# Kernel tuning notes

Measured on AMD Instinct MI355X. Metric: run time of the kernel, lower is better.

## Reference

```python
import jax, jax.numpy as jnp
import numpy as np
import math

B, MSA, L, D = 1, 64, 256, 512
H = 8
DH = D // H  # 64


def setup_inputs() -> dict:
    key = jax.random.key(0)
    ks = jax.random.split(key, 6)
    x = jax.random.normal(ks[0], (B, MSA, L, D), dtype=jnp.float32)
    Wq = jax.random.normal(ks[1], (D, D), dtype=jnp.float32) * (1.0 / math.sqrt(D))
    Wk = jax.random.normal(ks[2], (D, D), dtype=jnp.float32) * (1.0 / math.sqrt(D))
    Wv = jax.random.normal(ks[3], (D, D), dtype=jnp.float32) * (1.0 / math.sqrt(D))
    aK = jax.random.normal(ks[4], (L, L, DH), dtype=jnp.float32)
    aV = jax.random.normal(ks[5], (L, L, DH), dtype=jnp.float32)
    return {"x": x, "Wq": Wq, "Wk": Wk, "Wv": Wv, "aK": aK, "aV": aV}


def _proj(t, W, b, m, l, h, dh):
    # nn.Linear(bias=False): t @ W.T, then split heads -> (B,H,MSA,L,dh)
    y = jnp.einsum('bmld,ed->bmle', t, W).reshape(b, m, l, h, dh)
    return jnp.transpose(y, (0, 3, 1, 2, 4))


def reference(x, Wq, Wk, Wv, aK, aV):
    b, m, l, d = x.shape
    h, dh = H, DH
    q = _proj(x, Wq, b, m, l, h, dh)  # (B,H,MSA,L,dh)
    k = _proj(x, Wk, b, m, l, h, dh)
    v = _proj(x, Wv, b, m, l, h, dh)
    # content score + relative-position score
    e1 = jnp.einsum('bhmid,bhmjd->bhmij', q, k)           # (B,H,MSA,L,L)
    e2 = jnp.einsum('bhmid,ijd->bhmij', q, aK)            # (B,H,MSA,L,L)
    alpha = jax.nn.softmax((e1 + e2) / math.sqrt(dh), axis=-1)
    z1 = jnp.einsum('bhmij,bhmjd->bhmid', alpha, v)       # content output
    z2 = jnp.einsum('bhmij,ijd->bhmid', alpha, aV)        # relative-V output
    z = (z1 + z2).sum(axis=2)                             # sum over MSA -> (B,H,L,dh)
    out = jnp.transpose(z, (0, 2, 1, 3)).reshape(b, l, d) # (B,L,D)
    return out
```

## Files before the change

### kernel.cpp

```cpp
#include <hip/hip_runtime.h>

#define THREADS 256

typedef unsigned short u16;
typedef __attribute__((ext_vector_type(8))) short bf16x8;
typedef __attribute__((ext_vector_type(4))) float f32x4;

__device__ __forceinline__ u16 f2bf(float f) {
  unsigned int u = __float_as_uint(f);
  u += 0x7fffu + ((u >> 16) & 1u);
  return (u16)(u >> 16);
}
__device__ __forceinline__ float bf2f(u16 s) {
  return __uint_as_float(((unsigned int)s) << 16);
}
__device__ __forceinline__ bf16x8 ld8g(const u16* p) {
  return *reinterpret_cast<const bf16x8*>(p);
}
__device__ __forceinline__ bf16x8 ld8s(const u16* p) {
  return *reinterpret_cast<const bf16x8*>(p);
}
__device__ __forceinline__ void st4bf(u16* dst, float4 v) {
  unsigned int lo = (unsigned int)f2bf(v.x) | ((unsigned int)f2bf(v.y) << 16);
  unsigned int hi = (unsigned int)f2bf(v.z) | ((unsigned int)f2bf(v.w) << 16);
  uint2 u; u.x = lo; u.y = hi;
  *reinterpret_cast<uint2*>(dst) = u;
}
typedef __attribute__((address_space(1))) const unsigned int g_u32;
typedef __attribute__((address_space(3))) unsigned int l_u32;
__device__ __forceinline__ void async16(const u16* g, u16* l) {
  __builtin_amdgcn_global_load_lds((g_u32*)g, (l_u32*)l, 16, 0, 0);
}

__global__ __launch_bounds__(THREADS) void cast_xw(
    const float* __restrict__ x, const float* __restrict__ wq,
    const float* __restrict__ wk, const float* __restrict__ wv,
    const float* __restrict__ aK,
    u16* __restrict__ xb, u16* __restrict__ wqb, u16* __restrict__ wkb,
    u16* __restrict__ wvb, u16* __restrict__ aKb) {
  int t = blockIdx.x * THREADS + threadIdx.x;
  if (t < 2097152) {
    st4bf(xb + t * 4, reinterpret_cast<const float4*>(x)[t]);
  } else if (t < 2162688) {
    int q = t - 2097152;
    st4bf(wqb + q * 4, reinterpret_cast<const float4*>(wq)[q]);
  } else if (t < 2228224) {
    int q = t - 2162688;
    st4bf(wkb + q * 4, reinterpret_cast<const float4*>(wk)[q]);
  } else if (t < 2293760) {
    int q = t - 2228224;
    st4bf(wvb + q * 4, reinterpret_cast<const float4*>(wv)[q]);
  } else if (t < 3342336) {
    int q = t - 2293760;
    st4bf(aKb + q * 4, reinterpret_cast<const float4*>(aK)[q]);
  }
}

__global__ __launch_bounds__(THREADS) void proj_gemm(
    const u16* __restrict__ xb, const u16* __restrict__ wb,
    u16* __restrict__ qh, u16* __restrict__ kb, u16* __restrict__ vt) {
  const int bid = blockIdx.x;
  const int swzb = (bid & 7) * 192 + (bid >> 3);
  const int bm = swzb / 12, bn = swzb % 12;
  const int tid = threadIdx.x;
  const int wave = tid >> 6, lane = tid & 63;
  const int quad = lane >> 4, l15 = lane & 15;
  __shared__ __align__(16) u16 smem[9216];
  u16* At = smem;
  u16* Bt = smem + 4096;

  const int rowL = lane >> 2;
  const int chunkL = (lane & 3) ^ ((lane >> 3) & 3);
  const u16* gA = xb + (size_t)(bm * 128 + wave * 32 + rowL) * 512 + chunkL * 8;
  const u16* gB = wb + (size_t)(bn * 128 + wave * 32 + rowL) * 512 + chunkL * 8;
  u16* lA = At + wave * 1024;
  u16* lB = Bt + wave * 1024;

  const int rw0 = (wave & 1) * 64, cw0 = (wave >> 1) * 64;
  const int swz = (quad ^ ((l15 >> 1) & 3)) * 8;

  f32x4 acc[4][4];
#pragma unroll
  for (int mt = 0; mt < 4; ++mt)
#pragma unroll
    for (int nt = 0; nt < 4; ++nt) acc[mt][nt] = (f32x4){0.f, 0.f, 0.f, 0.f};

  for (int s = 0; s < 16; ++s) {
    __syncthreads();
    async16(gA + s * 32, lA);
    async16(gA + s * 32 + 8192, lA + 512);
    async16(gB + s * 32, lB);
    async16(gB + s * 32 + 8192, lB + 512);
    __syncthreads();
    bf16x8 af[4], bf[4];
#pragma unroll
    for (int mt = 0; mt < 4; ++mt)
      af[mt] = ld8s(At + (rw0 + mt * 16 + l15) * 32 + swz);
#pragma unroll
    for (int nt = 0; nt < 4; ++nt)
      bf[nt] = ld8s(Bt + (cw0 + nt * 16 + l15) * 32 + swz);
#pragma unroll
    for (int mt = 0; mt < 4; ++mt)
#pragma unroll
      for (int nt = 0; nt < 4; ++nt)
        acc[mt][nt] = __builtin_amdgcn_mfma_f32_16x16x32_bf16(af[mt], bf[nt], acc[mt][nt], 0, 0, 0);
  }

  const int mat = bn >> 2;
  const int h0 = (bn & 3) * 2;
  const int m = bm >> 1;
  const int l0 = (bm & 1) * 128;

  if (mat < 2) {
    u16* dstb = (mat == 0) ? qh : kb;
    const int il = tid >> 1, cc = (tid & 1) * 32;
#pragma unroll
    for (int p = 0; p < 2; ++p) {
      __syncthreads();
      if ((wave >> 1) == p) {
#pragma unroll
        for (int mt = 0; mt < 4; ++mt)
#pragma unroll
          for (int nt = 0; nt < 4; ++nt)
#pragma unroll
            for (int r = 0; r < 4; ++r)
              smem[(rw0 + mt * 16 + quad * 4 + r) * 72 + nt * 16 + l15] =
                  f2bf(acc[mt][nt][r]);
      }
      __syncthreads();
      u16* dst = dstb + ((size_t)((h0 + p) * 64 + m) * 256 + l0 + il) * 64 + cc;
      uint4 v0 = *reinterpret_cast<uint4*>(&smem[il * 72 + cc]);
      uint4 v1 = *reinterpret_cast<uint4*>(&smem[il * 72 + cc + 8]);
      uint4 v2 = *reinterpret_cast<uint4*>(&smem[il * 72 + cc + 16]);
      uint4 v3 = *reinterpret_cast<uint4*>(&smem[il * 72 + cc + 24]);
      *reinterpret_cast<uint4*>(dst) = v0;
      *reinterpret_cast<uint4*>(dst + 8) = v1;
      *reinterpret_cast<uint4*>(dst + 16) = v2;
      *reinterpret_cast<uint4*>(dst + 24) = v3;
    }
  } else {
    const int tl = tid >> 2, cc = (tid & 3) * 32;
#pragma unroll
    for (int p = 0; p < 2; ++p) {
      __syncthreads();
      if ((wave >> 1) == p) {
#pragma unroll
        for (int mt = 0; mt < 4; ++mt)
#pragma unroll
          for (int nt = 0; nt < 4; ++nt)
#pragma unroll
            for (int r = 0; r < 4; ++r)
              smem[(nt * 16 + l15) * 136 + rw0 + mt * 16 + quad * 4 + r] =
                  f2bf(acc[mt][nt][r]);
      }
      __syncthreads();
      int hm = (h0 + p) * 64 + m;
      u16* dst = vt + (size_t)hm * 16384 + tl * 256 + l0 + cc;
      uint4 v0 = *reinterpret_cast<uint4*>(&smem[tl * 136 + cc]);
      uint4 v1 = *reinterpret_cast<uint4*>(&smem[tl * 136 + cc + 8]);
      uint4 v2 = *reinterpret_cast<uint4*>(&smem[tl * 136 + cc + 16]);
      uint4 v3 = *reinterpret_cast<uint4*>(&smem[tl * 136 + cc + 24]);
      *reinterpret_cast<uint4*>(dst) = v0;
      *reinterpret_cast<uint4*>(dst + 8) = v1;
      *reinterpret_cast<uint4*>(dst + 16) = v2;
      *reinterpret_cast<uint4*>(dst + 24) = v3;
    }
  }
}

__global__ __launch_bounds__(THREADS) void e2_k(
    const u16* __restrict__ qh, const u16* __restrict__ aKb,
    u16* __restrict__ e2g) {
  const int hmt = blockIdx.x >> 8, i = blockIdx.x & 255;
  const int tid = threadIdx.x;
  const int wave = tid >> 6, lane = tid & 63;
  const int quad = lane >> 4, l15 = lane & 15;
  __shared__ u16 aKl[256 * 72];
  __shared__ u16 qL[64 * 72];
#pragma unroll
  for (int c = 0; c < 8; ++c) {
    int fidx = c * 2048 + tid * 8;
    int j = fidx >> 6, d = fidx & 63;
    uint4 v = *reinterpret_cast<const uint4*>(aKb + (size_t)i * 16384 + fidx);
    *reinterpret_cast<uint4*>(&aKl[j * 72 + d]) = v;
  }
#pragma unroll
  for (int c = 0; c < 4; ++c) {
    int r = c * 16 + (tid >> 4);
    int dd = (tid & 15) * 4;
    uint2 v = *reinterpret_cast<const uint2*>(
        qh + ((size_t)(hmt * 64 + r) * 256 + i) * 64 + dd);
    *reinterpret_cast<uint2*>(&qL[r * 72 + dd]) = v;
  }
  __syncthreads();
  f32x4 acc[16];
#pragma unroll
  for (int nt = 0; nt < 16; ++nt) acc[nt] = (f32x4){0.f, 0.f, 0.f, 0.f};
  bf16x8 a[2];
#pragma unroll
  for (int ks = 0; ks < 2; ++ks)
    a[ks] = ld8s(&qL[(wave * 16 + l15) * 72 + ks * 32 + quad * 8]);
#pragma unroll
  for (int nt = 0; nt < 16; ++nt) {
#pragma unroll
    for (int ks = 0; ks < 2; ++ks) {
      bf16x8 b = ld8s(&aKl[(nt * 16 + l15) * 72 + ks * 32 + quad * 8]);
      acc[nt] = __builtin_amdgcn_mfma_f32_16x16x32_bf16(a[ks], b, acc[nt], 0, 0, 0);
    }
  }
  __syncthreads();
  u16* S = aKl;
#pragma unroll
  for (int nt = 0; nt < 16; ++nt)
#pragma unroll
    for (int r = 0; r < 4; ++r)
      S[(wave * 16 + quad * 4 + r) * 264 + nt * 16 + l15] = f2bf(acc[nt][r]);
  __syncthreads();
#pragma unroll
  for (int c = 0; c < 8; ++c) {
    int lin = c * 2048 + tid * 8;
    int row = lin >> 8, col = lin & 255;
    uint4 v = *reinterpret_cast<uint4*>(&S[row * 264 + col]);
    *reinterpret_cast<uint4*>(e2g + ((size_t)(hmt * 64 + row) * 256 + i) * 256 + col) = v;
  }
}

__global__ __launch_bounds__(THREADS, 2) void attn_f(
    const u16* __restrict__ qh, const u16* __restrict__ kb,
    const u16* __restrict__ vt, const u16* __restrict__ e2g,
    u16* __restrict__ betap, u16* __restrict__ z1q) {
  const int bi = blockIdx.x;
  const int it = bi >> 7;
  const int hmc = bi & 127;
  const int h = hmc >> 4, mc = hmc & 15;
  const int tid = threadIdx.x;
  const int wave = tid >> 6, lane = tid & 63;
  const int quad = lane >> 4, l15 = lane & 15;
  __shared__ u16 As[4 * 4224];
  u16* W = &As[wave * 4224];
  const int i0 = it * 64 + wave * 16;

  f32x4 betaacc[16];
  f32x4 acc2[4];
#pragma unroll
  for (int nt = 0; nt < 16; ++nt) betaacc[nt] = (f32x4){0.f, 0.f, 0.f, 0.f};
#pragma unroll
  for (int nt = 0; nt < 4; ++nt) acc2[nt] = (f32x4){0.f, 0.f, 0.f, 0.f};

  for (int mi = 0; mi < 4; ++mi) {
    const int hm = h * 64 + mc * 4 + mi;
    f32x4 acc[16];
    const u16* e2p = e2g + ((size_t)hm * 256 + i0 + quad * 4) * 256 + l15;
#pragma unroll
    for (int nt = 0; nt < 16; ++nt)
#pragma unroll
      for (int r = 0; r < 4; ++r)
        acc[nt][r] = bf2f(e2p[r * 256 + nt * 16]);
    bf16x8 a[2];
#pragma unroll
    for (int ks = 0; ks < 2; ++ks)
      a[ks] = ld8g(qh + ((size_t)hm * 256 + i0 + l15) * 64 + ks * 32 + quad * 8);
#pragma unroll
    for (int nt = 0; nt < 16; ++nt) {
#pragma unroll
      for (int ks = 0; ks < 2; ++ks) {
        bf16x8 b = ld8g(kb + ((size_t)hm * 256 + nt * 16 + l15) * 64 + ks * 32 + quad * 8);
        acc[nt] = __builtin_amdgcn_mfma_f32_16x16x32_bf16(a[ks], b, acc[nt], 0, 0, 0);
      }
    }
#pragma unroll
    for (int r = 0; r < 4; ++r) {
      float s = 0.f;
#pragma unroll
      for (int nt = 0; nt < 16; ++nt) {
        float p = __expf(acc[nt][r] * 0.125f);
        acc[nt][r] = p;
        s += p;
      }
      for (int msk = 1; msk < 16; msk <<= 1) s += __shfl_xor(s, msk);
      float inv = 1.0f / s;
      int lrow = quad * 4 + r;
#pragma unroll
      for (int nt = 0; nt < 16; ++nt) {
        float av = acc[nt][r] * inv;
        betaacc[nt][r] += av;
        W[lrow * 264 + nt * 16 + l15] = f2bf(av);
      }
    }
#pragma unroll
    for (int ks = 0; ks < 8; ++ks) {
      bf16x8 a2 = ld8s(&W[l15 * 264 + ks * 32 + quad * 8]);
#pragma unroll
      for (int nt = 0; nt < 4; ++nt) {
        bf16x8 b2 = ld8g(vt + (size_t)hm * 16384 + (nt * 16 + l15) * 256 + ks * 32 + quad * 8);
        acc2[nt] = __builtin_amdgcn_mfma_f32_16x16x32_bf16(a2, b2, acc2[nt], 0, 0, 0);
      }
    }
  }

#pragma unroll
  for (int nt = 0; nt < 16; ++nt)
#pragma unroll
    for (int r = 0; r < 4; ++r)
      W[(quad * 4 + r) * 264 + nt * 16 + l15] = f2bf(betaacc[nt][r]);
#pragma unroll
  for (int c = 0; c < 8; ++c) {
    int lin = c * 512 + lane * 8;
    int row = lin >> 8, col = lin & 255;
    uint4 v = *reinterpret_cast<uint4*>(&W[row * 264 + col]);
    *reinterpret_cast<uint4*>(
        betap + ((size_t)hmc * 256 + it * 64 + wave * 16 + row) * 256 + col) = v;
  }
#pragma unroll
  for (int nt = 0; nt < 4; ++nt)
#pragma unroll
    for (int r = 0; r < 4; ++r)
      W[(quad * 4 + r) * 72 + nt * 16 + l15] = f2bf(acc2[nt][r]);
  {
    int row = lane >> 2, col = (lane & 3) * 16;
    uint4 v0 = *reinterpret_cast<uint4*>(&W[row * 72 + col]);
    uint4 v1 = *reinterpret_cast<uint4*>(&W[row * 72 + col + 8]);
    u16* dst = z1q + ((size_t)hmc * 256 + it * 64 + wave * 16 + row) * 64 + col;
    *reinterpret_cast<uint4*>(dst) = v0;
    *reinterpret_cast<uint4*>(dst + 8) = v1;
  }
}

__global__ __launch_bounds__(THREADS) void z2f_k(
    const u16* __restrict__ betap, const u16* __restrict__ z1q,
    const float* __restrict__ aV, float* __restrict__ out) {
  const int i = blockIdx.x;
  const int tid = threadIdx.x;
  const int wave = tid >> 6, lane = tid & 63;
  const int quad = lane >> 4, l15 = lane & 15;
  __shared__ u16 aVl[64 * 264];
  __shared__ float bj[8 * 256];
  __shared__ float z2L[512];
#pragma unroll
  for (int c = 0; c < 8; ++c) {
    int fidx = c * 2048 + tid * 8;
    int j = fidx >> 6, d = fidx & 63;
    float4 f0 = *reinterpret_cast<const float4*>(aV + (size_t)i * 16384 + fidx);
    float4 f1 = *reinterpret_cast<const float4*>(aV + (size_t)i * 16384 + fidx + 4);
    float fv[8] = {f0.x, f0.y, f0.z, f0.w, f1.x, f1.y, f1.z, f1.w};
#pragma unroll
    for (int u = 0; u < 8; ++u) aVl[(d + u) * 264 + j] = f2bf(fv[u]);
  }
  {
    int h = tid >> 5, j0 = (tid & 31) * 8;
    const u16* src = betap + (size_t)(h * 16) * 65536 + i * 256 + j0;
    float s[8] = {0.f, 0.f, 0.f, 0.f, 0.f, 0.f, 0.f, 0.f};
#pragma unroll
    for (int m = 0; m < 16; ++m) {
      uint4 v = *reinterpret_cast<const uint4*>(src + (size_t)m * 65536);
      const u16* pv = reinterpret_cast<const u16*>(&v);
#pragma unroll
      for (int u = 0; u < 8; ++u) s[u] += bf2f(pv[u]);
    }
#pragma unroll
    for (int u = 0; u < 8; ++u) bj[h * 256 + j0 + u] = s[u];
  }
  __syncthreads();
  f32x4 acc = (f32x4){0.f, 0.f, 0.f, 0.f};
#pragma unroll
  for (int ks = 0; ks < 8; ++ks) {
    u16 ab[8];
    if (l15 < 8) {
      const float* bp = &bj[l15 * 256 + ks * 32 + quad * 8];
#pragma unroll
      for (int u = 0; u < 8; ++u) ab[u] = f2bf(bp[u]);
    } else {
#pragma unroll
      for (int u = 0; u < 8; ++u) ab[u] = 0;
    }
    bf16x8 a = *reinterpret_cast<bf16x8*>(ab);
    bf16x8 b = ld8s(&aVl[(wave * 16 + l15) * 264 + ks * 32 + quad * 8]);
    acc = __builtin_amdgcn_mfma_f32_16x16x32_bf16(a, b, acc, 0, 0, 0);
  }
#pragma unroll
  for (int r = 0; r < 4; ++r) {
    int hh = quad * 4 + r;
    if (hh < 8) z2L[hh * 64 + wave * 16 + l15] = acc[r];
  }
  __syncthreads();
#pragma unroll
  for (int c = 0; c < 2; ++c) {
    int e = c * 256 + tid;
    int h = e >> 6, d = e & 63;
    float s = z2L[e];
    const u16* base = z1q + ((size_t)(h * 16) * 256 + i) * 64 + d;
#pragma unroll
    for (int m = 0; m < 16; ++m) s += bf2f(base[(size_t)m * 16384]);
    out[(size_t)i * 512 + e] = s;
  }
}

extern "C" void kernel_launch(void* const* d_in, const int* in_sizes, int n_in,
                              void* d_out, int out_size, void* d_ws, size_t ws_size,
                              hipStream_t stream) {
  const float* x  = (const float*)d_in[0];
  const float* wq = (const float*)d_in[1];
  const float* wk = (const float*)d_in[2];
  const float* wv = (const float*)d_in[3];
  const float* aK = (const float*)d_in[4];
  const float* aV = (const float*)d_in[5];
  float* out = (float*)d_out;

  char* ws = (char*)d_ws;
  u16* xb    = (u16*)(ws + 0);
  u16* wqb   = (u16*)(ws + 16777216);
  u16* wkb   = (u16*)(ws + 17301504);
  u16* wvb   = (u16*)(ws + 17825792);
  u16* betap = (u16*)(ws + 18350080);
  u16* qh    = (u16*)(ws + 35127296);
  u16* kb    = (u16*)(ws + 51904512);
  u16* vt    = (u16*)(ws + 68681728);
  u16* e2g   = (u16*)(ws + 85458944);
  u16* aKb   = (u16*)(ws + 152567808);
  u16* z1q   = xb;

  cast_xw<<<13056, THREADS, 0, stream>>>(x, wq, wk, wv, aK, xb, wqb, wkb, wvb, aKb);
  proj_gemm<<<1536, THREADS, 0, stream>>>(xb, wqb, qh, kb, vt);
  e2_k<<<2048, THREADS, 0, stream>>>(qh, aKb, e2g);
  attn_f<<<512, THREADS, 0, stream>>>(qh, kb, vt, e2g, betap, z1q);
  z2f_k<<<256, THREADS, 0, stream>>>(betap, z1q, aV, out);
}
```

Before: 256.4 us.

## Reuse aK tile across four hm tiles in e2 kernel with transposed Q copy

```diff
diff --git a/kernel.cpp b/kernel.cpp
--- a/kernel.cpp
+++ b/kernel.cpp
@@ -58,7 +58,8 @@
 
 __global__ __launch_bounds__(THREADS) void proj_gemm(
     const u16* __restrict__ xb, const u16* __restrict__ wb,
-    u16* __restrict__ qh, u16* __restrict__ kb, u16* __restrict__ vt) {
+    u16* __restrict__ qh, u16* __restrict__ qT,
+    u16* __restrict__ kb, u16* __restrict__ vt) {
   const int bid = blockIdx.x;
   const int swzb = (bid & 7) * 192 + (bid >> 3);
   const int bm = swzb / 12, bn = swzb % 12;
@@ -128,7 +129,8 @@
                   f2bf(acc[mt][nt][r]);
       }
       __syncthreads();
-      u16* dst = dstb + ((size_t)((h0 + p) * 64 + m) * 256 + l0 + il) * 64 + cc;
+      int hm = (h0 + p) * 64 + m;
+      u16* dst = dstb + ((size_t)hm * 256 + l0 + il) * 64 + cc;
       uint4 v0 = *reinterpret_cast<uint4*>(&smem[il * 72 + cc]);
       uint4 v1 = *reinterpret_cast<uint4*>(&smem[il * 72 + cc + 8]);
       uint4 v2 = *reinterpret_cast<uint4*>(&smem[il * 72 + cc + 16]);
@@ -137,6 +139,13 @@
       *reinterpret_cast<uint4*>(dst + 8) = v1;
       *reinterpret_cast<uint4*>(dst + 16) = v2;
       *reinterpret_cast<uint4*>(dst + 24) = v3;
+      if (mat == 0) {
+        u16* dstT = qT + ((size_t)(l0 + il) * 512 + hm) * 64 + cc;
+        *reinterpret_cast<uint4*>(dstT) = v0;
+        *reinterpret_cast<uint4*>(dstT + 8) = v1;
+        *reinterpret_cast<uint4*>(dstT + 16) = v2;
+        *reinterpret_cast<uint4*>(dstT + 24) = v3;
+      }
     }
   } else {
     const int tl = tid >> 2, cc = (tid & 3) * 32;
@@ -169,59 +178,62 @@
 }
 
 __global__ __launch_bounds__(THREADS) void e2_k(
-    const u16* __restrict__ qh, const u16* __restrict__ aKb,
+    const u16* __restrict__ qT, const u16* __restrict__ aKb,
     u16* __restrict__ e2g) {
-  const int hmt = blockIdx.x >> 8, i = blockIdx.x & 255;
+  const int hmt2 = blockIdx.x >> 8, i = blockIdx.x & 255;
+  const int hm0 = hmt2 * 256;
   const int tid = threadIdx.x;
   const int wave = tid >> 6, lane = tid & 63;
   const int quad = lane >> 4, l15 = lane & 15;
-  __shared__ u16 aKl[256 * 72];
-  __shared__ u16 qL[64 * 72];
+  __shared__ __align__(16) u16 aKl[256 * 64];
+  __shared__ __align__(16) u16 stg[4][16 * 256];
+  char* aKc = reinterpret_cast<char*>(aKl);
 #pragma unroll
   for (int c = 0; c < 8; ++c) {
-    int fidx = c * 2048 + tid * 8;
-    int j = fidx >> 6, d = fidx & 63;
-    uint4 v = *reinterpret_cast<const uint4*>(aKb + (size_t)i * 16384 + fidx);
-    *reinterpret_cast<uint4*>(&aKl[j * 72 + d]) = v;
-  }
-#pragma unroll
-  for (int c = 0; c < 4; ++c) {
-    int r = c * 16 + (tid >> 4);
-    int dd = (tid & 15) * 4;
-    uint2 v = *reinterpret_cast<const uint2*>(
-        qh + ((size_t)(hmt * 64 + r) * 256 + i) * 64 + dd);
-    *reinterpret_cast<uint2*>(&qL[r * 72 + dd]) = v;
+    int chunk = c * 256 + tid;
+    int j = chunk >> 3;
+    int d2 = (chunk & 7) * 8;
+    uint4 v = *reinterpret_cast<const uint4*>(aKb + (size_t)i * 16384 + j * 64 + d2);
+    *reinterpret_cast<uint4*>(aKc + j * 128 + ((d2 * 2) ^ ((j & 7) << 4))) = v;
   }
   __syncthreads();
-  f32x4 acc[16];
-#pragma unroll
-  for (int nt = 0; nt < 16; ++nt) acc[nt] = (f32x4){0.f, 0.f, 0.f, 0.f};
-  bf16x8 a[2];
-#pragma unroll
-  for (int ks = 0; ks < 2; ++ks)
-    a[ks] = ld8s(&qL[(wave * 16 + l15) * 72 + ks * 32 + quad * 8]);
-#pragma unroll
-  for (int nt = 0; nt < 16; ++nt) {
-#pragma unroll
-    for (int ks = 0; ks < 2; ++ks) {
-      bf16x8 b = ld8s(&aKl[(nt * 16 + l15) * 72 + ks * 32 + quad * 8]);
-      acc[nt] = __builtin_amdgcn_mfma_f32_16x16x32_bf16(a[ks], b, acc[nt], 0, 0, 0);
-    }
-  }
-  __syncthreads();
-  u16* S = aKl;
-#pragma unroll
-  for (int nt = 0; nt < 16; ++nt)
-#pragma unroll
-    for (int r = 0; r < 4; ++r)
-      S[(wave * 16 + quad * 4 + r) * 264 + nt * 16 + l15] = f2bf(acc[nt][r]);
-  __syncthreads();
-#pragma unroll
-  for (int c = 0; c < 8; ++c) {
-    int lin = c * 2048 + tid * 8;
-    int row = lin >> 8, col = lin & 255;
-    uint4 v = *reinterpret_cast<uint4*>(&S[row * 264 + col]);
-    *reinterpret_cast<uint4*>(e2g + ((size_t)(hmt * 64 + row) * 256 + i) * 256 + col) = v;
+  char* W2 = reinterpret_cast<char*>(stg[wave]);
+  for (int mt = 0; mt < 4; ++mt) {
+    const int hmr = hm0 + mt * 64 + wave * 16;
+    bf16x8 a[2];
+#pragma unroll
+    for (int ks = 0; ks < 2; ++ks)
+      a[ks] = ld8g(qT + ((size_t)i * 512 + hmr + l15) * 64 + ks * 32 + quad * 8);
+    f32x4 acc[16];
+#pragma unroll
+    for (int nt = 0; nt < 16; ++nt) acc[nt] = (f32x4){0.f, 0.f, 0.f, 0.f};
+#pragma unroll
+    for (int nt = 0; nt < 16; ++nt) {
+      int j = nt * 16 + l15;
+#pragma unroll
+      for (int ks = 0; ks < 2; ++ks) {
+        bf16x8 b = *reinterpret_cast<const bf16x8*>(
+            aKc + j * 128 + ((ks * 64 + quad * 16) ^ ((j & 7) << 4)));
+        acc[nt] = __builtin_amdgcn_mfma_f32_16x16x32_bf16(a[ks], b, acc[nt], 0, 0, 0);
+      }
+    }
+#pragma unroll
+    for (int nt = 0; nt < 16; ++nt)
+#pragma unroll
+      for (int r = 0; r < 4; ++r) {
+        int row = quad * 4 + r, col = nt * 16 + l15;
+        *reinterpret_cast<u16*>(W2 + row * 512 + ((col * 2) ^ ((row & 7) << 4))) =
+            f2bf(acc[nt][r]);
+      }
+#pragma unroll
+    for (int c = 0; c < 8; ++c) {
+      int lin = c * 512 + lane * 8;
+      int row = lin >> 8, col = lin & 255;
+      uint4 v = *reinterpret_cast<uint4*>(
+          W2 + row * 512 + ((col * 2) ^ ((row & 7) << 4)));
+      *reinterpret_cast<uint4*>(
+          e2g + ((size_t)(hmr + row) * 256 + i) * 256 + col) = v;
+    }
   }
 }
 
@@ -412,6 +424,7 @@
   u16* wkb   = (u16*)(ws + 17301504);
   u16* wvb   = (u16*)(ws + 17825792);
   u16* betap = (u16*)(ws + 18350080);
+  u16* qT    = betap;
   u16* qh    = (u16*)(ws + 35127296);
   u16* kb    = (u16*)(ws + 51904512);
   u16* vt    = (u16*)(ws + 68681728);
@@ -420,8 +433,8 @@
   u16* z1q   = xb;
 
   cast_xw<<<13056, THREADS, 0, stream>>>(x, wq, wk, wv, aK, xb, wqb, wkb, wvb, aKb);
-  proj_gemm<<<1536, THREADS, 0, stream>>>(xb, wqb, qh, kb, vt);
-  e2_k<<<2048, THREADS, 0, stream>>>(qh, aKb, e2g);
+  proj_gemm<<<1536, THREADS, 0, stream>>>(xb, wqb, qh, qT, kb, vt);
+  e2_k<<<512, THREADS, 0, stream>>>(qT, aKb, e2g);
   attn_f<<<512, THREADS, 0, stream>>>(qh, kb, vt, e2g, betap, z1q);
   z2f_k<<<256, THREADS, 0, stream>>>(betap, z1q, aV, out);
 }
```

New measurement: 262.6 us. 2.4% more time.

## Split attention per MSA row and move the MSA reduction into final kernel

Applied to the files above, without the earlier changes.

```diff
diff --git a/kernel.cpp b/kernel.cpp
--- a/kernel.cpp
+++ b/kernel.cpp
@@ -225,14 +225,13 @@
   }
 }
 
-__global__ __launch_bounds__(THREADS, 2) void attn_f(
+__global__ __launch_bounds__(THREADS, 4) void attn_f(
     const u16* __restrict__ qh, const u16* __restrict__ kb,
-    const u16* __restrict__ vt, const u16* __restrict__ e2g,
-    u16* __restrict__ betap, u16* __restrict__ z1q) {
+    const u16* __restrict__ vt, u16* __restrict__ e2g,
+    u16* __restrict__ z1q) {
   const int bi = blockIdx.x;
-  const int it = bi >> 7;
-  const int hmc = bi & 127;
-  const int h = hmc >> 4, mc = hmc & 15;
+  const int it = bi >> 9;
+  const int hm = bi & 511;
   const int tid = threadIdx.x;
   const int wave = tid >> 6, lane = tid & 63;
   const int quad = lane >> 4, l15 = lane & 15;
@@ -240,76 +239,60 @@
   u16* W = &As[wave * 4224];
   const int i0 = it * 64 + wave * 16;
 
-  f32x4 betaacc[16];
-  f32x4 acc2[4];
-#pragma unroll
-  for (int nt = 0; nt < 16; ++nt) betaacc[nt] = (f32x4){0.f, 0.f, 0.f, 0.f};
-#pragma unroll
-  for (int nt = 0; nt < 4; ++nt) acc2[nt] = (f32x4){0.f, 0.f, 0.f, 0.f};
-
-  for (int mi = 0; mi < 4; ++mi) {
-    const int hm = h * 64 + mc * 4 + mi;
-    f32x4 acc[16];
-    const u16* e2p = e2g + ((size_t)hm * 256 + i0 + quad * 4) * 256 + l15;
+  f32x4 acc[16];
+  const u16* e2p = e2g + ((size_t)hm * 256 + i0 + quad * 4) * 256 + l15;
+#pragma unroll
+  for (int nt = 0; nt < 16; ++nt)
+#pragma unroll
+    for (int r = 0; r < 4; ++r)
+      acc[nt][r] = bf2f(e2p[r * 256 + nt * 16]);
+  bf16x8 a[2];
+#pragma unroll
+  for (int ks = 0; ks < 2; ++ks)
+    a[ks] = ld8g(qh + ((size_t)hm * 256 + i0 + l15) * 64 + ks * 32 + quad * 8);
+#pragma unroll
+  for (int nt = 0; nt < 16; ++nt) {
+#pragma unroll
+    for (int ks = 0; ks < 2; ++ks) {
+      bf16x8 b = ld8g(kb + ((size_t)hm * 256 + nt * 16 + l15) * 64 + ks * 32 + quad * 8);
+      acc[nt] = __builtin_amdgcn_mfma_f32_16x16x32_bf16(a[ks], b, acc[nt], 0, 0, 0);
+    }
+  }
+#pragma unroll
+  for (int r = 0; r < 4; ++r) {
+    float s = 0.f;
+#pragma unroll
+    for (int nt = 0; nt < 16; ++nt) {
+      float p = __expf(acc[nt][r] * 0.125f);
+      acc[nt][r] = p;
+      s += p;
+    }
+    for (int msk = 1; msk < 16; msk <<= 1) s += __shfl_xor(s, msk);
+    float inv = 1.0f / s;
+    int lrow = quad * 4 + r;
 #pragma unroll
     for (int nt = 0; nt < 16; ++nt)
-#pragma unroll
-      for (int r = 0; r < 4; ++r)
-        acc[nt][r] = bf2f(e2p[r * 256 + nt * 16]);
-    bf16x8 a[2];
-#pragma unroll
-    for (int ks = 0; ks < 2; ++ks)
-      a[ks] = ld8g(qh + ((size_t)hm * 256 + i0 + l15) * 64 + ks * 32 + quad * 8);
-#pragma unroll
-    for (int nt = 0; nt < 16; ++nt) {
-#pragma unroll
-      for (int ks = 0; ks < 2; ++ks) {
-        bf16x8 b = ld8g(kb + ((size_t)hm * 256 + nt * 16 + l15) * 64 + ks * 32 + quad * 8);
-        acc[nt] = __builtin_amdgcn_mfma_f32_16x16x32_bf16(a[ks], b, acc[nt], 0, 0, 0);
-      }
-    }
-#pragma unroll
-    for (int r = 0; r < 4; ++r) {
-      float s = 0.f;
-#pragma unroll
-      for (int nt = 0; nt < 16; ++nt) {
-        float p = __expf(acc[nt][r] * 0.125f);
-        acc[nt][r] = p;
-        s += p;
-      }
-      for (int msk = 1; msk < 16; msk <<= 1) s += __shfl_xor(s, msk);
-      float inv = 1.0f / s;
-      int lrow = quad * 4 + r;
-#pragma unroll
-      for (int nt = 0; nt < 16; ++nt) {
-        float av = acc[nt][r] * inv;
-        betaacc[nt][r] += av;
-        W[lrow * 264 + nt * 16 + l15] = f2bf(av);
-      }
-    }
-#pragma unroll
-    for (int ks = 0; ks < 8; ++ks) {
-      bf16x8 a2 = ld8s(&W[l15 * 264 + ks * 32 + quad * 8]);
-#pragma unroll
-      for (int nt = 0; nt < 4; ++nt) {
-        bf16x8 b2 = ld8g(vt + (size_t)hm * 16384 + (nt * 16 + l15) * 256 + ks * 32 + quad * 8);
-        acc2[nt] = __builtin_amdgcn_mfma_f32_16x16x32_bf16(a2, b2, acc2[nt], 0, 0, 0);
-      }
-    }
-  }
-
-#pragma unroll
-  for (int nt = 0; nt < 16; ++nt)
-#pragma unroll
-    for (int r = 0; r < 4; ++r)
-      W[(quad * 4 + r) * 264 + nt * 16 + l15] = f2bf(betaacc[nt][r]);
+      W[lrow * 264 + nt * 16 + l15] = f2bf(acc[nt][r] * inv);
+  }
 #pragma unroll
   for (int c = 0; c < 8; ++c) {
     int lin = c * 512 + lane * 8;
     int row = lin >> 8, col = lin & 255;
     uint4 v = *reinterpret_cast<uint4*>(&W[row * 264 + col]);
     *reinterpret_cast<uint4*>(
-        betap + ((size_t)hmc * 256 + it * 64 + wave * 16 + row) * 256 + col) = v;
+        e2g + ((size_t)hm * 256 + i0 + row) * 256 + col) = v;
+  }
+  f32x4 acc2[4];
+#pragma unroll
+  for (int nt = 0; nt < 4; ++nt) acc2[nt] = (f32x4){0.f, 0.f, 0.f, 0.f};
+#pragma unroll
+  for (int ks = 0; ks < 8; ++ks) {
+    bf16x8 a2 = ld8s(&W[l15 * 264 + ks * 32 + quad * 8]);
+#pragma unroll
+    for (int nt = 0; nt < 4; ++nt) {
+      bf16x8 b2 = ld8g(vt + (size_t)hm * 16384 + (nt * 16 + l15) * 256 + ks * 32 + quad * 8);
+      acc2[nt] = __builtin_amdgcn_mfma_f32_16x16x32_bf16(a2, b2, acc2[nt], 0, 0, 0);
+    }
   }
 #pragma unroll
   for (int nt = 0; nt < 4; ++nt)
@@ -320,14 +303,14 @@
     int row = lane >> 2, col = (lane & 3) * 16;
     uint4 v0 = *reinterpret_cast<uint4*>(&W[row * 72 + col]);
     uint4 v1 = *reinterpret_cast<uint4*>(&W[row * 72 + col + 8]);
-    u16* dst = z1q + ((size_t)hmc * 256 + it * 64 + wave * 16 + row) * 64 + col;
+    u16* dst = z1q + ((size_t)hm * 256 + i0 + row) * 64 + col;
     *reinterpret_cast<uint4*>(dst) = v0;
     *reinterpret_cast<uint4*>(dst + 8) = v1;
   }
 }
 
 __global__ __launch_bounds__(THREADS) void z2f_k(
-    const u16* __restrict__ betap, const u16* __restrict__ z1q,
+    const u16* __restrict__ alphag, const u16* __restrict__ z1q,
     const float* __restrict__ aV, float* __restrict__ out) {
   const int i = blockIdx.x;
   const int tid = threadIdx.x;
@@ -348,10 +331,10 @@
   }
   {
     int h = tid >> 5, j0 = (tid & 31) * 8;
-    const u16* src = betap + (size_t)(h * 16) * 65536 + i * 256 + j0;
+    const u16* src = alphag + (size_t)(h * 64) * 65536 + i * 256 + j0;
     float s[8] = {0.f, 0.f, 0.f, 0.f, 0.f, 0.f, 0.f, 0.f};
-#pragma unroll
-    for (int m = 0; m < 16; ++m) {
+#pragma unroll 8
+    for (int m = 0; m < 64; ++m) {
       uint4 v = *reinterpret_cast<const uint4*>(src + (size_t)m * 65536);
       const u16* pv = reinterpret_cast<const u16*>(&v);
 #pragma unroll
@@ -388,9 +371,9 @@
     int e = c * 256 + tid;
     int h = e >> 6, d = e & 63;
     float s = z2L[e];
-    const u16* base = z1q + ((size_t)(h * 16) * 256 + i) * 64 + d;
-#pragma unroll
-    for (int m = 0; m < 16; ++m) s += bf2f(base[(size_t)m * 16384]);
+    const u16* base = z1q + ((size_t)(h * 64) * 256 + i) * 64 + d;
+#pragma unroll 8
+    for (int m = 0; m < 64; ++m) s += bf2f(base[(size_t)m * 16384]);
     out[(size_t)i * 512 + e] = s;
   }
 }
@@ -411,7 +394,6 @@
   u16* wqb   = (u16*)(ws + 16777216);
   u16* wkb   = (u16*)(ws + 17301504);
   u16* wvb   = (u16*)(ws + 17825792);
-  u16* betap = (u16*)(ws + 18350080);
   u16* qh    = (u16*)(ws + 35127296);
   u16* kb    = (u16*)(ws + 51904512);
   u16* vt    = (u16*)(ws + 68681728);
@@ -422,6 +404,6 @@
   cast_xw<<<13056, THREADS, 0, stream>>>(x, wq, wk, wv, aK, xb, wqb, wkb, wvb, aKb);
   proj_gemm<<<1536, THREADS, 0, stream>>>(xb, wqb, qh, kb, vt);
   e2_k<<<2048, THREADS, 0, stream>>>(qh, aKb, e2g);
-  attn_f<<<512, THREADS, 0, stream>>>(qh, kb, vt, e2g, betap, z1q);
-  z2f_k<<<256, THREADS, 0, stream>>>(betap, z1q, aV, out);
-}
+  attn_f<<<2048, THREADS, 0, stream>>>(qh, kb, vt, e2g, z1q);
+  z2f_k<<<256, THREADS, 0, stream>>>(e2g, z1q, aV, out);
+}
```

Result: slower. 263.7 us (+2.8%).
